# Performance work log

Measured on AMD Instinct MI355X. Metric: run time of the kernel, lower is better.

Reference implementation:

```python
import jax, jax.numpy as jnp
import numpy as np

EMB = 1024
HEADS = 16
HEAD_DIM = EMB // HEADS
EPS = 1e-5


def layer_norm(x, scale, shift):
    mean = jnp.mean(x, axis=-1, keepdims=True)
    var = jnp.mean(jnp.square(x - mean), axis=-1, keepdims=True)  # unbiased=False
    return scale * ((x - mean) / jnp.sqrt(var + EPS)) + shift


def gelu_tanh(x):
    c = jnp.sqrt(jnp.asarray(2.0 / jnp.pi, x.dtype))
    return 0.5 * x * (1.0 + jnp.tanh(c * (x + 0.044715 * x * x * x)))


def setup_inputs() -> dict:
    key = jax.random.key(0)
    ks = jax.random.split(key, 12)
    s = 0.02
    B, S, D = 2, 2048, EMB
    return {
        "x": jax.random.normal(ks[0], (B, S, D), jnp.float32),
        "wq": jax.random.normal(ks[1], (D, D), jnp.float32) * s,
        "wk": jax.random.normal(ks[2], (D, D), jnp.float32) * s,
        "wv": jax.random.normal(ks[3], (D, D), jnp.float32) * s,
        "wo": jax.random.normal(ks[4], (D, D), jnp.float32) * s,
        "bo": jnp.zeros((D,), jnp.float32),
        "w1": jax.random.normal(ks[5], (D, 4 * D), jnp.float32) * s,
        "b1": jnp.zeros((4 * D,), jnp.float32),
        "w2": jax.random.normal(ks[6], (4 * D, D), jnp.float32) * s,
        "b2": jnp.zeros((D,), jnp.float32),
        "g1": jnp.ones((D,), jnp.float32),
        "s1": jnp.zeros((D,), jnp.float32),
        "g2": jnp.ones((D,), jnp.float32),
        "s2": jnp.zeros((D,), jnp.float32),
    }


def reference(x, wq, wk, wv, wo, bo, w1, b1, w2, b2, g1, s1, g2, s2):
    B, S, D = x.shape
    # --- attention sub-block ---
    h = layer_norm(x, g1, s1)
    q = (h @ wq).reshape(B, S, HEADS, HEAD_DIM).transpose(0, 2, 1, 3)  # [B,H,S,d]
    k = (h @ wk).reshape(B, S, HEADS, HEAD_DIM).transpose(0, 2, 1, 3)
    v = (h @ wv).reshape(B, S, HEADS, HEAD_DIM).transpose(0, 2, 1, 3)
    scores = jnp.einsum("bhqd,bhkd->bhqk", q, k)
    causal = jnp.tril(jnp.ones((S, S), bool))  # True = keep
    scores = jnp.where(causal, scores, -jnp.inf)
    attn = jax.nn.softmax(scores / jnp.sqrt(jnp.asarray(HEAD_DIM, x.dtype)), axis=-1)
    ctx = jnp.einsum("bhqk,bhkd->bhqd", attn, v).transpose(0, 2, 1, 3).reshape(B, S, D)
    x = x + (ctx @ wo + bo)
    # --- FFN sub-block ---
    h = layer_norm(x, g2, s2)
    h = gelu_tanh(h @ w1 + b1) @ w2 + b2
    return x + h
```

## Files before the change

kernel.cpp:

```cpp
#include <hip/hip_runtime.h>


typedef __attribute__((ext_vector_type(8))) short s16x8;
typedef __attribute__((ext_vector_type(4))) float f32x4;
typedef __attribute__((ext_vector_type(16))) float f32x16;
typedef unsigned short u16;
typedef unsigned int u32;

#define DEV static __device__ __forceinline__
#define MFMA16 __builtin_amdgcn_mfma_f32_16x16x32_bf16
#define MFMA32 __builtin_amdgcn_mfma_f32_32x32x16_bf16
#define GLOAD_LDS16(gp, lp)                                         \
  __builtin_amdgcn_global_load_lds(                                 \
      (const __attribute__((address_space(1))) void*)(gp),          \
      (__attribute__((address_space(3))) void*)(lp), 16, 0, 0)

DEV u16 f2bf(float f) {
  union { float f; unsigned u; } c; c.f = f;
  unsigned u = c.u;
  u += 0x7fff + ((u >> 16) & 1);
  return (u16)(u >> 16);
}

DEV u32 cvtpk(float lo, float hi) {
  u32 r;
  asm("v_cvt_pk_bf16_f32 %0, %1, %2" : "=v"(r) : "v"(lo), "v"(hi));
  return r;
}

DEV float gelu_tanh(float v) {
  const float c0 = 0.7978845608028654f;
  float u = c0 * (v + 0.044715f * v * v * v);
  return 0.5f * v * (1.0f + tanhf(u));
}

DEV s16x8 ld8(const u16* p) { return *(const s16x8*)p; }

__global__ __launch_bounds__(256) void tconv_kernel(
    const float* __restrict__ W, u16* __restrict__ Wt, int K, int N) {
  __shared__ u16 T[64][80];
  const int t = threadIdx.x;
  const int n0 = blockIdx.x * 64, k0 = blockIdx.y * 64;
  const int kr = t >> 4, nc = (t & 15) * 4;
#pragma unroll
  for (int p = 0; p < 4; ++p) {
    const int k = p * 16 + kr;
    float4 v = *(const float4*)(W + (size_t)(k0 + k) * N + n0 + nc);
    T[nc + 0][k] = f2bf(v.x);
    T[nc + 1][k] = f2bf(v.y);
    T[nc + 2][k] = f2bf(v.z);
    T[nc + 3][k] = f2bf(v.w);
  }
  __syncthreads();
  const int nr = t >> 2, kc = (t & 3) * 16;
  *(s16x8*)(Wt + (size_t)(n0 + nr) * K + k0 + kc) = *(const s16x8*)&T[nr][kc];
  *(s16x8*)(Wt + (size_t)(n0 + nr) * K + k0 + kc + 8) =
      *(const s16x8*)&T[nr][kc + 8];
}

__global__ __launch_bounds__(256) void ln_kernel(
    const float* __restrict__ x, const float* __restrict__ g,
    const float* __restrict__ b, u16* __restrict__ out) {
  const int row = blockIdx.x;
  const int t = threadIdx.x;
  const float* xr = x + (size_t)row * 1024;
  float4 v = *(const float4*)(xr + t * 4);
  float s = v.x + v.y + v.z + v.w;
  float ss = v.x * v.x + v.y * v.y + v.z * v.z + v.w * v.w;
#pragma unroll
  for (int off = 1; off < 64; off <<= 1) {
    s += __shfl_xor(s, off);
    ss += __shfl_xor(ss, off);
  }
  __shared__ float sb[4], ssb[4];
  const int w = t >> 6;
  if ((t & 63) == 0) { sb[w] = s; ssb[w] = ss; }
  __syncthreads();
  s = sb[0] + sb[1] + sb[2] + sb[3];
  ss = ssb[0] + ssb[1] + ssb[2] + ssb[3];
  const float mean = s * (1.0f / 1024.0f);
  const float var = ss * (1.0f / 1024.0f) - mean * mean;
  const float rstd = rsqrtf(var + 1e-5f);
  const int c = t * 4;
  ushort4 o;
  o.x = f2bf(g[c + 0] * ((v.x - mean) * rstd) + b[c + 0]);
  o.y = f2bf(g[c + 1] * ((v.y - mean) * rstd) + b[c + 1]);
  o.z = f2bf(g[c + 2] * ((v.z - mean) * rstd) + b[c + 2]);
  o.w = f2bf(g[c + 3] * ((v.w - mean) * rstd) + b[c + 3]);
  *(ushort4*)(out + (size_t)row * 1024 + c) = o;
}

DEV void gemm_stage(const u16* __restrict__ A, const u16* __restrict__ Bt,
                    int bm, int bn, int K, int kof, u16 (*Al)[32],
                    u16 (*Bl)[32], int w, int lane) {
  const int srow = lane >> 2;
  const int scol = ((lane & 3) ^ ((lane >> 3) & 3)) * 8;
#pragma unroll
  for (int p = 0; p < 2; ++p) {
    const int r0 = (w * 2 + p) * 16;
    GLOAD_LDS16(A + (size_t)(bm + r0 + srow) * K + kof + scol, &Al[r0][0]);
    GLOAD_LDS16(Bt + (size_t)(bn + r0 + srow) * K + kof + scol, &Bl[r0][0]);
  }
}

DEV void gemm_step(const u16 (*Al)[32], const u16 (*Bl)[32],
                   f32x4 (&acc)[4][4], int wm, int wn, int lr, int lg) {
  const int cs = (lg ^ ((lr >> 1) & 3)) * 8;
  s16x8 af[4], bf[4];
#pragma unroll
  for (int i = 0; i < 4; ++i) {
    af[i] = *(const s16x8*)&Al[wm + i * 16 + lr][cs];
    bf[i] = *(const s16x8*)&Bl[wn + i * 16 + lr][cs];
  }
#pragma unroll
  for (int i = 0; i < 4; ++i)
#pragma unroll
    for (int j = 0; j < 4; ++j)
      acc[i][j] = MFMA16(af[i], bf[j], acc[i][j], 0, 0, 0);
}

template <int EPI>
__global__ __launch_bounds__(256) void gemm_kernel(
    const u16* __restrict__ A, const u16* __restrict__ Bt,
    const float* __restrict__ bias, const float* __restrict__ res,
    void* __restrict__ Cv, int M, int N, int K) {
  __shared__ __align__(16) u16 Al[2][128][32];
  __shared__ __align__(16) u16 Bl[2][128][32];
  const int t = threadIdx.x;
  const int lane = t & 63, w = t >> 6;
  const int wm = (w >> 1) * 64, wn = (w & 1) * 64;
  int bid = blockIdx.y * gridDim.x + blockIdx.x;
  const int q8 = (gridDim.x * gridDim.y) >> 3;
  bid = (bid & 7) * q8 + (bid >> 3);
  const int bm = (bid / gridDim.x) * 128, bn = (bid % gridDim.x) * 128;
  const int lr = lane & 15, lg = lane >> 4;
  f32x4 acc[4][4] = {};
  const int nkt = K >> 5;

  gemm_stage(A, Bt, bm, bn, K, 0, Al[0], Bl[0], w, lane);
  __syncthreads();
  for (int kt = 0; kt < nkt - 1; ++kt) {
    const int cur = kt & 1;
    gemm_stage(A, Bt, bm, bn, K, (kt + 1) << 5, Al[cur ^ 1], Bl[cur ^ 1], w,
               lane);
    gemm_step(Al[cur], Bl[cur], acc, wm, wn, lr, lg);
    __syncthreads();
  }
  gemm_step(Al[(nkt - 1) & 1], Bl[(nkt - 1) & 1], acc, wm, wn, lr, lg);

#pragma unroll
  for (int i = 0; i < 4; ++i) {
    const int row = bm + wm + i * 16 + lg * 4;
#pragma unroll
    for (int j = 0; j < 4; ++j) {
      const int col = bn + wn + j * 16 + lr;
      if (EPI == 0) {
        const int bb = row >> 11, sloc = row & 2047;
        const int which = col >> 10, n = col & 1023;
        const int hh = n >> 6, dd = n & 63;
        u16* qbuf = (u16*)Cv;
        if (which == 2) {
          ushort4 o;
          o.x = f2bf(acc[i][j][0]); o.y = f2bf(acc[i][j][1]);
          o.z = f2bf(acc[i][j][2]); o.w = f2bf(acc[i][j][3]);
          *(ushort4*)(qbuf + 8388608 +
                      (size_t)((bb * 16 + hh) * 64 + dd) * 2048 + sloc) = o;
        } else {
          const float sc = (which == 0) ? 0.18033688011112042f : 1.0f;
          u16* dst = qbuf + (size_t)which * 4194304 +
                     ((size_t)(bb * 16 + hh) * 2048 + sloc) * 64 + dd;
#pragma unroll
          for (int e = 0; e < 4; ++e) dst[(size_t)e * 64] = f2bf(acc[i][j][e] * sc);
        }
      } else if (EPI == 1) {
        float* C = (float*)Cv;
        const float bs = bias[col];
#pragma unroll
        for (int e = 0; e < 4; ++e)
          C[(size_t)(row + e) * N + col] =
              acc[i][j][e] + bs + res[(size_t)(row + e) * N + col];
      } else {
        u16* C = (u16*)Cv;
        const float bs = bias[col];
#pragma unroll
        for (int e = 0; e < 4; ++e)
          C[(size_t)(row + e) * N + col] = f2bf(gelu_tanh(acc[i][j][e] + bs));
      }
    }
  }
}

DEV void g64_stage(const u16* __restrict__ A, const u16* __restrict__ Bt,
                   int bm, int bn, int K, int kof, u16 (*Al)[32],
                   u16 (*Bl)[32], int w, int lane) {
  const int srow = lane >> 2;
  const int scol = ((lane & 3) ^ ((lane >> 3) & 3)) * 8;
  const int r0 = w << 4;
  GLOAD_LDS16(A + (size_t)(bm + r0 + srow) * K + kof + scol, &Al[r0][0]);
  GLOAD_LDS16(Bt + (size_t)(bn + r0 + srow) * K + kof + scol, &Bl[r0][0]);
}

DEV void g64_step(const u16 (*Al)[32], const u16 (*Bl)[32],
                  f32x4 (&acc)[2][2], int wm, int wn, int lr, int lg) {
  const int cs = (lg ^ ((lr >> 1) & 3)) * 8;
  s16x8 af[2], bf[2];
#pragma unroll
  for (int i = 0; i < 2; ++i) {
    af[i] = *(const s16x8*)&Al[wm + i * 16 + lr][cs];
    bf[i] = *(const s16x8*)&Bl[wn + i * 16 + lr][cs];
  }
#pragma unroll
  for (int i = 0; i < 2; ++i)
#pragma unroll
    for (int j = 0; j < 2; ++j)
      acc[i][j] = MFMA16(af[i], bf[j], acc[i][j], 0, 0, 0);
}

template <int EPI>
__global__ __launch_bounds__(256) void gemm64_kernel(
    const u16* __restrict__ A, const u16* __restrict__ Bt,
    const float* __restrict__ bias, const float* __restrict__ res,
    void* __restrict__ Cv, int M, int N, int K) {
  __shared__ __align__(16) u16 Al[2][64][32];
  __shared__ __align__(16) u16 Bl[2][64][32];
  const int t = threadIdx.x;
  const int lane = t & 63, w = t >> 6;
  const int wm = (w >> 1) * 32, wn = (w & 1) * 32;
  int bid = blockIdx.y * gridDim.x + blockIdx.x;
  const int q8 = (gridDim.x * gridDim.y) >> 3;
  bid = (bid & 7) * q8 + (bid >> 3);
  const int bm = (bid / gridDim.x) * 64, bn = (bid % gridDim.x) * 64;
  const int lr = lane & 15, lg = lane >> 4;
  f32x4 acc[2][2] = {};
  const int nkt = K >> 5;

  g64_stage(A, Bt, bm, bn, K, 0, Al[0], Bl[0], w, lane);
  __syncthreads();
  for (int kt = 0; kt < nkt - 1; ++kt) {
    const int cur = kt & 1;
    g64_stage(A, Bt, bm, bn, K, (kt + 1) << 5, Al[cur ^ 1], Bl[cur ^ 1], w,
              lane);
    g64_step(Al[cur], Bl[cur], acc, wm, wn, lr, lg);
    __syncthreads();
  }
  g64_step(Al[(nkt - 1) & 1], Bl[(nkt - 1) & 1], acc, wm, wn, lr, lg);

#pragma unroll
  for (int i = 0; i < 2; ++i) {
    const int row = bm + wm + i * 16 + lg * 4;
#pragma unroll
    for (int j = 0; j < 2; ++j) {
      const int col = bn + wn + j * 16 + lr;
      if (EPI == 1) {
        float* C = (float*)Cv;
        const float bs = bias[col];
#pragma unroll
        for (int e = 0; e < 4; ++e)
          C[(size_t)(row + e) * N + col] =
              acc[i][j][e] + bs + res[(size_t)(row + e) * N + col];
      } else {
        u16* C = (u16*)Cv;
        const float bs = bias[col];
#pragma unroll
        for (int e = 0; e < 4; ++e)
          C[(size_t)(row + e) * N + col] = f2bf(gelu_tanh(acc[i][j][e] + bs));
      }
    }
  }
}

DEV void g256_stage(const u16* __restrict__ A, const u16* __restrict__ Bt,
                    int bm, int bn, int K, int kof, u16 (*Al)[32],
                    u16 (*Bl)[32], int w, int lane) {
  const int srow = lane >> 2;
  const int scol = ((lane & 3) ^ ((lane >> 3) & 3)) * 8;
#pragma unroll
  for (int c = 0; c < 2; ++c) {
    const int r0 = (w << 5) + (c << 4);
    GLOAD_LDS16(A + (size_t)(bm + r0 + srow) * K + kof + scol, &Al[r0][0]);
    GLOAD_LDS16(Bt + (size_t)(bn + r0 + srow) * K + kof + scol, &Bl[r0][0]);
  }
}

DEV void g256_step(const u16 (*Al)[32], const u16 (*Bl)[32],
                   f32x4 (&acc)[8][4], int wm, int wn, int lr, int lg) {
  const int cs = (lg ^ ((lr >> 1) & 3)) * 8;
  s16x8 af[8], bf[4];
#pragma unroll
  for (int i = 0; i < 8; ++i)
    af[i] = *(const s16x8*)&Al[wm + i * 16 + lr][cs];
#pragma unroll
  for (int j = 0; j < 4; ++j)
    bf[j] = *(const s16x8*)&Bl[wn + j * 16 + lr][cs];
#pragma unroll
  for (int i = 0; i < 8; ++i)
#pragma unroll
    for (int j = 0; j < 4; ++j)
      acc[i][j] = MFMA16(af[i], bf[j], acc[i][j], 0, 0, 0);
}

template <int EPI>
__global__ __launch_bounds__(512, 2) void gemm256_kernel(
    const u16* __restrict__ A, const u16* __restrict__ Bt,
    const float* __restrict__ bias, const float* __restrict__ res,
    void* __restrict__ Cv, int M, int N, int K) {
  __shared__ __align__(16) u16 Al[2][256][32];
  __shared__ __align__(16) u16 Bl[2][256][32];
  const int t = threadIdx.x;
  const int lane = t & 63, w = t >> 6;
  const int wm = (w >> 2) << 7;
  const int wn = (w & 3) << 6;
  int bid = blockIdx.y * gridDim.x + blockIdx.x;
  const int q8 = (gridDim.x * gridDim.y) >> 3;
  bid = (bid & 7) * q8 + (bid >> 3);
  const int bm = (bid / gridDim.x) << 8, bn = (bid % gridDim.x) << 8;
  const int lr = lane & 15, lg = lane >> 4;
  f32x4 acc[8][4] = {};
  const int nkt = K >> 5;

  g256_stage(A, Bt, bm, bn, K, 0, Al[0], Bl[0], w, lane);
  __syncthreads();
  for (int kt = 0; kt < nkt - 1; ++kt) {
    const int cur = kt & 1;
    g256_stage(A, Bt, bm, bn, K, (kt + 1) << 5, Al[cur ^ 1], Bl[cur ^ 1], w,
               lane);
    g256_step(Al[cur], Bl[cur], acc, wm, wn, lr, lg);
    __syncthreads();
  }
  g256_step(Al[(nkt - 1) & 1], Bl[(nkt - 1) & 1], acc, wm, wn, lr, lg);

#pragma unroll
  for (int i = 0; i < 8; ++i) {
    const int row = bm + wm + i * 16 + lg * 4;
#pragma unroll
    for (int j = 0; j < 4; ++j) {
      const int col = bn + wn + j * 16 + lr;
      if (EPI == 1) {
        float* C = (float*)Cv;
        const float bs = bias[col];
#pragma unroll
        for (int e = 0; e < 4; ++e)
          C[(size_t)(row + e) * N + col] =
              acc[i][j][e] + bs + res[(size_t)(row + e) * N + col];
      } else {
        u16* C = (u16*)Cv;
        const float bs = bias[col];
#pragma unroll
        for (int e = 0; e < 4; ++e)
          C[(size_t)(row + e) * N + col] = f2bf(gelu_tanh(acc[i][j][e] + bs));
      }
    }
  }
}

DEV float vmax16(const f32x16& v) {
  float a = fmaxf(v[0], v[1]), b = fmaxf(v[2], v[3]);
  float c = fmaxf(v[4], v[5]), d = fmaxf(v[6], v[7]);
  float e = fmaxf(v[8], v[9]), f = fmaxf(v[10], v[11]);
  float g = fmaxf(v[12], v[13]), h = fmaxf(v[14], v[15]);
  a = fmaxf(a, b); c = fmaxf(c, d); e = fmaxf(e, f); g = fmaxf(g, h);
  return fmaxf(fmaxf(a, c), fmaxf(e, g));
}
DEV float vsum16(const f32x16& v) {
  float a = v[0] + v[1], b = v[2] + v[3];
  float c = v[4] + v[5], d = v[6] + v[7];
  float e = v[8] + v[9], f = v[10] + v[11];
  float g = v[12] + v[13], h = v[14] + v[15];
  a += b; c += d; e += f; g += h;
  return (a + c) + (e + g);
}

struct A32 {
  s16x8 q[4];
  f32x16 o0, o1;
  float m, l;
};

template <int MODE>
DEV void body32(A32& st, int k0, const u16* Kb, const u16* Vb, int la,
                int hi) {
  s16x8 ka0[4], ka1[4];
#pragma unroll
  for (int c = 0; c < 4; ++c)
    ka0[c] = ld8(Kb + (size_t)(k0 + la) * 64 + c * 16 + hi * 8);
  if (MODE != 2)
#pragma unroll
    for (int c = 0; c < 4; ++c)
      ka1[c] = ld8(Kb + (size_t)(k0 + 32 + la) * 64 + c * 16 + hi * 8);
  f32x16 s0, s1;
#pragma unroll
  for (int r = 0; r < 16; ++r) { s0[r] = 0.f; s1[r] = 0.f; }
#pragma unroll
  for (int c = 0; c < 4; ++c) s0 = MFMA32(ka0[c], st.q[c], s0, 0, 0, 0);
  if (MODE != 2)
#pragma unroll
    for (int c = 0; c < 4; ++c) s1 = MFMA32(ka1[c], st.q[c], s1, 0, 0, 0);
  const int nkc = (MODE == 2) ? 2 : 4;
  s16x8 va0[4], va1[4];
#pragma unroll
  for (int kc = 0; kc < 4; ++kc)
    if (kc < nkc) {
      va0[kc] = ld8(Vb + (size_t)la * 2048 + k0 + kc * 16 + hi * 8);
      va1[kc] = ld8(Vb + (size_t)(32 + la) * 2048 + k0 + kc * 16 + hi * 8);
    }
  if (MODE == 1) {
#pragma unroll
    for (int r = 0; r < 16; ++r) {
      const int kl = (r & 3) + 8 * (r >> 2) + 4 * hi;
      if (kl > la) s1[r] = -INFINITY;
    }
  }
  if (MODE == 2) {
#pragma unroll
    for (int r = 0; r < 16; ++r) {
      const int kl = (r & 3) + 8 * (r >> 2) + 4 * hi;
      if (kl > la) s0[r] = -INFINITY;
    }
  }
  float mt = vmax16(s0);
  if (MODE != 2) mt = fmaxf(mt, vmax16(s1));
  mt = fmaxf(mt, __shfl_xor(mt, 32));
  const float mn = fmaxf(st.m, mt);
  const float sf = exp2f(st.m - mn);
#pragma unroll
  for (int r = 0; r < 16; ++r) s0[r] = exp2f(s0[r] - mn);
  if (MODE != 2)
#pragma unroll
    for (int r = 0; r < 16; ++r) s1[r] = exp2f(s1[r] - mn);
  float rs = vsum16(s0);
  if (MODE != 2) rs += vsum16(s1);
  rs += __shfl_xor(rs, 32);
  st.l = st.l * sf + rs;
  st.m = mn;
#pragma unroll
  for (int r = 0; r < 16; ++r) { st.o0[r] *= sf; st.o1[r] *= sf; }
  const int nh = (MODE == 2) ? 1 : 2;
#pragma unroll
  for (int half = 0; half < nh; ++half) {
    u32 w[8];
#pragma unroll
    for (int i = 0; i < 8; ++i)
      w[i] = half ? cvtpk(s1[2 * i], s1[2 * i + 1])
                  : cvtpk(s0[2 * i], s0[2 * i + 1]);
#pragma unroll
    for (int kp = 0; kp < 2; ++kp) {
      const u32 w0 = w[4 * kp + 0], w1 = w[4 * kp + 1];
      const u32 w2 = w[4 * kp + 2], w3 = w[4 * kp + 3];
      const u32 t0 = hi ? w0 : w2, t1 = hi ? w1 : w3;
      const u32 x0 = (u32)__shfl_xor((int)t0, 32);
      const u32 x1 = (u32)__shfl_xor((int)t1, 32);
      union { u32 u[4]; s16x8 v; } bb;
      bb.u[0] = hi ? x0 : w0;
      bb.u[1] = hi ? x1 : w1;
      bb.u[2] = hi ? w2 : x0;
      bb.u[3] = hi ? w3 : x1;
      const int kc = half * 2 + kp;
      st.o0 = MFMA32(va0[kc], bb.v, st.o0, 0, 0, 0);
      st.o1 = MFMA32(va1[kc], bb.v, st.o1, 0, 0, 0);
    }
  }
}

DEV void a32_init(A32& st, const u16* Qbase, int qs, int la, int hi) {
#pragma unroll
  for (int c = 0; c < 4; ++c)
    st.q[c] = ld8(Qbase + (size_t)(qs + la) * 64 + c * 16 + hi * 8);
#pragma unroll
  for (int r = 0; r < 16; ++r) { st.o0[r] = 0.f; st.o1[r] = 0.f; }
  st.m = -INFINITY;
  st.l = 0.f;
}

DEV void a32_fin(const A32& st, u16* __restrict__ ctx, int bh, int qs, int la,
                 int hi) {
  const int bb = bh >> 4, hh = bh & 15;
  const float inv = 1.0f / st.l;
  u16* crow = ctx + (size_t)(bb * 2048 + qs + la) * 1024 + hh * 64;
#pragma unroll
  for (int r = 0; r < 16; r += 2) {
    const int d = (r & 3) + 8 * (r >> 2) + 4 * hi;
    *(u32*)(crow + d) = cvtpk(st.o0[r] * inv, st.o0[r + 1] * inv);
    *(u32*)(crow + 32 + d) = cvtpk(st.o1[r] * inv, st.o1[r + 1] * inv);
  }
}

template <bool ODD>
DEV void chain_tail(A32& st, int nfull, int qs, const u16* Kb, const u16* Vb,
                    int la, int hi) {
  if (ODD) body32<1>(st, nfull * 64, Kb, Vb, la, hi);
  else     body32<2>(st, qs, Kb, Vb, la, hi);
}

__global__ __launch_bounds__(64) void attn_kernel(
    const u16* __restrict__ Qg, const u16* __restrict__ Kg,
    const u16* __restrict__ Vt, u16* __restrict__ ctx) {
  const int lane = threadIdx.x & 63;
  const int la = lane & 31, hi = lane >> 5;
  const int tA = blockIdx.x;
  const int bh = blockIdx.y;
  const int tB = 63 - tA;
  const int qsA = tA * 32, qsB = tB * 32;
  const int nfA = tA >> 1, nfB = tB >> 1;
  const size_t baseK = (size_t)bh * 2048 * 64;
  const size_t baseV = (size_t)bh * 64 * 2048;
  const u16* Kb = Kg + baseK;
  const u16* Vb = Vt + baseV;

  A32 A, B;
  a32_init(A, Qg + baseK, qsA, la, hi);
  a32_init(B, Qg + baseK, qsB, la, hi);

  for (int kt = 0; kt < nfA; ++kt) {
    body32<0>(B, kt * 64, Kb, Vb, la, hi);
    body32<0>(A, kt * 64, Kb, Vb, la, hi);
  }
  body32<0>(B, nfA * 64, Kb, Vb, la, hi);
  if (tA & 1) chain_tail<true>(A, nfA, qsA, Kb, Vb, la, hi);
  else        chain_tail<false>(A, nfA, qsA, Kb, Vb, la, hi);
  a32_fin(A, ctx, bh, qsA, la, hi);

  for (int kt = nfA + 1; kt < nfB; ++kt)
    body32<0>(B, kt * 64, Kb, Vb, la, hi);
  if (tB & 1) chain_tail<true>(B, nfB, qsB, Kb, Vb, la, hi);
  else        chain_tail<false>(B, nfB, qsB, Kb, Vb, la, hi);
  a32_fin(B, ctx, bh, qsB, la, hi);
}

extern "C" void kernel_launch(void* const* d_in, const int* in_sizes, int n_in,
                              void* d_out, int out_size, void* d_ws,
                              size_t ws_size, hipStream_t stream) {
  const float* x  = (const float*)d_in[0];
  const float* wq = (const float*)d_in[1];
  const float* wk = (const float*)d_in[2];
  const float* wv = (const float*)d_in[3];
  const float* wo = (const float*)d_in[4];
  const float* bo = (const float*)d_in[5];
  const float* w1 = (const float*)d_in[6];
  const float* b1 = (const float*)d_in[7];
  const float* w2 = (const float*)d_in[8];
  const float* b2 = (const float*)d_in[9];
  const float* g1 = (const float*)d_in[10];
  const float* s1 = (const float*)d_in[11];
  const float* g2 = (const float*)d_in[12];
  const float* s2 = (const float*)d_in[13];
  float* out = (float*)d_out;

  const size_t MB = (size_t)1 << 20;
  char* p = (char*)d_ws;
  u16* hb    = (u16*)(p + 0 * MB);
  u16* qbuf  = (u16*)(p + 8 * MB);
  u16* ctxb  = (u16*)(p + 32 * MB);
  float* x2  = (float*)(p + 40 * MB);
  u16* h2b   = (u16*)(p + 56 * MB);
  u16* qkvw  = (u16*)(p + 64 * MB);
  u16* wot   = (u16*)(p + 70 * MB);
  u16* w1t   = (u16*)(p + 72 * MB);
  u16* w2t   = (u16*)(p + 80 * MB);
  u16* gb    = (u16*)(p + 0 * MB);

  const dim3 blk(256);
  tconv_kernel<<<dim3(16, 16), blk, 0, stream>>>(wq, qkvw, 1024, 1024);
  tconv_kernel<<<dim3(16, 16), blk, 0, stream>>>(wk, qkvw + 1048576, 1024, 1024);
  tconv_kernel<<<dim3(16, 16), blk, 0, stream>>>(wv, qkvw + 2097152, 1024, 1024);
  tconv_kernel<<<dim3(16, 16), blk, 0, stream>>>(wo, wot, 1024, 1024);
  tconv_kernel<<<dim3(64, 16), blk, 0, stream>>>(w1, w1t, 1024, 4096);
  tconv_kernel<<<dim3(16, 64), blk, 0, stream>>>(w2, w2t, 4096, 1024);

  ln_kernel<<<4096, blk, 0, stream>>>(x, g1, s1, hb);
  gemm_kernel<0><<<dim3(24, 32), blk, 0, stream>>>(hb, qkvw, nullptr, nullptr,
                                                   qbuf, 4096, 3072, 1024);
  attn_kernel<<<dim3(32, 32), dim3(64), 0, stream>>>(
      qbuf, qbuf + 4194304, qbuf + 8388608, ctxb);
  gemm64_kernel<1><<<dim3(16, 64), blk, 0, stream>>>(ctxb, wot, bo, x, x2,
                                                     4096, 1024, 1024);
  ln_kernel<<<4096, blk, 0, stream>>>(x2, g2, s2, h2b);
  gemm256_kernel<2><<<dim3(16, 16), dim3(512), 0, stream>>>(
      h2b, w1t, b1, nullptr, gb, 4096, 4096, 1024);
  gemm64_kernel<1><<<dim3(16, 64), blk, 0, stream>>>(gb, w2t, b2, x2, out,
                                                     4096, 1024, 4096);
}
```

Baseline: 302.5 us.

## Triple-buffer GEMM pipelines, merge weight conversions, lazy softmax rescale

```diff
diff --git a/kernel.cpp b/kernel.cpp
--- a/kernel.cpp
+++ b/kernel.cpp
@@ -14,6 +14,7 @@
   __builtin_amdgcn_global_load_lds(                                 \
       (const __attribute__((address_space(1))) void*)(gp),          \
       (__attribute__((address_space(3))) void*)(lp), 16, 0, 0)
+#define WAIT_VM(N) asm volatile("s_waitcnt vmcnt(" #N ")" ::: "memory")
 
 DEV u16 f2bf(float f) {
   union { float f; unsigned u; } c; c.f = f;
@@ -36,11 +37,10 @@
 
 DEV s16x8 ld8(const u16* p) { return *(const s16x8*)p; }
 
-__global__ __launch_bounds__(256) void tconv_kernel(
-    const float* __restrict__ W, u16* __restrict__ Wt, int K, int N) {
+DEV void tconv_tile(const float* __restrict__ W, u16* __restrict__ Wt, int K,
+                    int N, int bx, int by, int t) {
   __shared__ u16 T[64][80];
-  const int t = threadIdx.x;
-  const int n0 = blockIdx.x * 64, k0 = blockIdx.y * 64;
+  const int n0 = bx * 64, k0 = by * 64;
   const int kr = t >> 4, nc = (t & 15) * 4;
 #pragma unroll
   for (int p = 0; p < 4; ++p) {
@@ -56,6 +56,29 @@
   *(s16x8*)(Wt + (size_t)(n0 + nr) * K + k0 + kc) = *(const s16x8*)&T[nr][kc];
   *(s16x8*)(Wt + (size_t)(n0 + nr) * K + k0 + kc + 8) =
       *(const s16x8*)&T[nr][kc + 8];
+}
+
+__global__ __launch_bounds__(256) void tconv_all(
+    const float* __restrict__ wq, const float* __restrict__ wk,
+    const float* __restrict__ wv, const float* __restrict__ wo,
+    const float* __restrict__ w1, const float* __restrict__ w2,
+    u16* __restrict__ qkvw, u16* __restrict__ wot, u16* __restrict__ w1t,
+    u16* __restrict__ w2t) {
+  const int idx = blockIdx.x, t = threadIdx.x;
+  if (idx < 768) {
+    const int which = idx >> 8, r = idx & 255;
+    const float* W = which == 0 ? wq : (which == 1 ? wk : wv);
+    tconv_tile(W, qkvw + which * 1048576, 1024, 1024, r & 15, r >> 4, t);
+  } else if (idx < 1024) {
+    const int r = idx - 768;
+    tconv_tile(wo, wot, 1024, 1024, r & 15, r >> 4, t);
+  } else if (idx < 2048) {
+    const int r = idx - 1024;
+    tconv_tile(w1, w1t, 1024, 4096, r & 63, r >> 6, t);
+  } else {
+    const int r = idx - 2048;
+    tconv_tile(w2, w2t, 4096, 1024, r & 15, r >> 4, t);
+  }
 }
 
 __global__ __launch_bounds__(256) void ln_kernel(
@@ -90,9 +113,9 @@
   *(ushort4*)(out + (size_t)row * 1024 + c) = o;
 }
 
-DEV void gemm_stage(const u16* __restrict__ A, const u16* __restrict__ Bt,
-                    int bm, int bn, int K, int kof, u16 (*Al)[32],
-                    u16 (*Bl)[32], int w, int lane) {
+DEV void stage128(const u16* __restrict__ A, const u16* __restrict__ Bt,
+                  int bm, int bn, int K, int kof, u16 (*Al)[32],
+                  u16 (*Bl)[32], int w, int lane) {
   const int srow = lane >> 2;
   const int scol = ((lane & 3) ^ ((lane >> 3) & 3)) * 8;
 #pragma unroll
@@ -103,8 +126,8 @@
   }
 }
 
-DEV void gemm_step(const u16 (*Al)[32], const u16 (*Bl)[32],
-                   f32x4 (&acc)[4][4], int wm, int wn, int lr, int lg) {
+DEV void step128(const u16 (*Al)[32], const u16 (*Bl)[32],
+                 f32x4 (&acc)[4][4], int wm, int wn, int lr, int lg) {
   const int cs = (lg ^ ((lr >> 1) & 3)) * 8;
   s16x8 af[4], bf[4];
 #pragma unroll
@@ -120,12 +143,12 @@
 }
 
 template <int EPI>
-__global__ __launch_bounds__(256) void gemm_kernel(
+__global__ __launch_bounds__(256) void pipe128_kernel(
     const u16* __restrict__ A, const u16* __restrict__ Bt,
     const float* __restrict__ bias, const float* __restrict__ res,
     void* __restrict__ Cv, int M, int N, int K) {
-  __shared__ __align__(16) u16 Al[2][128][32];
-  __shared__ __align__(16) u16 Bl[2][128][32];
+  __shared__ __align__(16) u16 Al[3][128][32];
+  __shared__ __align__(16) u16 Bl[3][128][32];
   const int t = threadIdx.x;
   const int lane = t & 63, w = t >> 6;
   const int wm = (w >> 1) * 64, wn = (w & 1) * 64;
@@ -137,16 +160,18 @@
   f32x4 acc[4][4] = {};
   const int nkt = K >> 5;
 
-  gemm_stage(A, Bt, bm, bn, K, 0, Al[0], Bl[0], w, lane);
-  __syncthreads();
-  for (int kt = 0; kt < nkt - 1; ++kt) {
-    const int cur = kt & 1;
-    gemm_stage(A, Bt, bm, bn, K, (kt + 1) << 5, Al[cur ^ 1], Bl[cur ^ 1], w,
-               lane);
-    gemm_step(Al[cur], Bl[cur], acc, wm, wn, lr, lg);
-    __syncthreads();
-  }
-  gemm_step(Al[(nkt - 1) & 1], Bl[(nkt - 1) & 1], acc, wm, wn, lr, lg);
+  stage128(A, Bt, bm, bn, K, 0, Al[0], Bl[0], w, lane);
+  stage128(A, Bt, bm, bn, K, 32, Al[1], Bl[1], w, lane);
+  for (int kt = 0; kt < nkt; ++kt) {
+    if (kt == nkt - 1) WAIT_VM(0);
+    else               WAIT_VM(4);
+    __builtin_amdgcn_s_barrier();
+    if (kt + 2 < nkt) {
+      const int nb = (kt + 2) % 3;
+      stage128(A, Bt, bm, bn, K, (kt + 2) << 5, Al[nb], Bl[nb], w, lane);
+    }
+    step128(Al[kt % 3], Bl[kt % 3], acc, wm, wn, lr, lg);
+  }
 
 #pragma unroll
   for (int i = 0; i < 4; ++i) {
@@ -172,13 +197,6 @@
 #pragma unroll
           for (int e = 0; e < 4; ++e) dst[(size_t)e * 64] = f2bf(acc[i][j][e] * sc);
         }
-      } else if (EPI == 1) {
-        float* C = (float*)Cv;
-        const float bs = bias[col];
-#pragma unroll
-        for (int e = 0; e < 4; ++e)
-          C[(size_t)(row + e) * N + col] =
-              acc[i][j][e] + bs + res[(size_t)(row + e) * N + col];
       } else {
         u16* C = (u16*)Cv;
         const float bs = bias[col];
@@ -190,9 +208,9 @@
   }
 }
 
-DEV void g64_stage(const u16* __restrict__ A, const u16* __restrict__ Bt,
-                   int bm, int bn, int K, int kof, u16 (*Al)[32],
-                   u16 (*Bl)[32], int w, int lane) {
+DEV void stage64(const u16* __restrict__ A, const u16* __restrict__ Bt,
+                 int bm, int bn, int K, int kof, u16 (*Al)[32],
+                 u16 (*Bl)[32], int w, int lane) {
   const int srow = lane >> 2;
   const int scol = ((lane & 3) ^ ((lane >> 3) & 3)) * 8;
   const int r0 = w << 4;
@@ -200,8 +218,8 @@
   GLOAD_LDS16(Bt + (size_t)(bn + r0 + srow) * K + kof + scol, &Bl[r0][0]);
 }
 
-DEV void g64_step(const u16 (*Al)[32], const u16 (*Bl)[32],
-                  f32x4 (&acc)[2][2], int wm, int wn, int lr, int lg) {
+DEV void step64(const u16 (*Al)[32], const u16 (*Bl)[32],
+                f32x4 (&acc)[2][2], int wm, int wn, int lr, int lg) {
   const int cs = (lg ^ ((lr >> 1) & 3)) * 8;
   s16x8 af[2], bf[2];
 #pragma unroll
@@ -216,13 +234,12 @@
       acc[i][j] = MFMA16(af[i], bf[j], acc[i][j], 0, 0, 0);
 }
 
-template <int EPI>
-__global__ __launch_bounds__(256) void gemm64_kernel(
+__global__ __launch_bounds__(256) void pipe64_kernel(
     const u16* __restrict__ A, const u16* __restrict__ Bt,
     const float* __restrict__ bias, const float* __restrict__ res,
-    void* __restrict__ Cv, int M, int N, int K) {
-  __shared__ __align__(16) u16 Al[2][64][32];
-  __shared__ __align__(16) u16 Bl[2][64][32];
+    float* __restrict__ C, int M, int N, int K) {
+  __shared__ __align__(16) u16 Al[3][64][32];
+  __shared__ __align__(16) u16 Bl[3][64][32];
   const int t = threadIdx.x;
   const int lane = t & 63, w = t >> 6;
   const int wm = (w >> 1) * 32, wn = (w & 1) * 32;
@@ -234,16 +251,18 @@
   f32x4 acc[2][2] = {};
   const int nkt = K >> 5;
 
-  g64_stage(A, Bt, bm, bn, K, 0, Al[0], Bl[0], w, lane);
-  __syncthreads();
-  for (int kt = 0; kt < nkt - 1; ++kt) {
-    const int cur = kt & 1;
-    g64_stage(A, Bt, bm, bn, K, (kt + 1) << 5, Al[cur ^ 1], Bl[cur ^ 1], w,
-              lane);
-    g64_step(Al[cur], Bl[cur], acc, wm, wn, lr, lg);
-    __syncthreads();
-  }
-  g64_step(Al[(nkt - 1) & 1], Bl[(nkt - 1) & 1], acc, wm, wn, lr, lg);
+  stage64(A, Bt, bm, bn, K, 0, Al[0], Bl[0], w, lane);
+  stage64(A, Bt, bm, bn, K, 32, Al[1], Bl[1], w, lane);
+  for (int kt = 0; kt < nkt; ++kt) {
+    if (kt == nkt - 1) WAIT_VM(0);
+    else               WAIT_VM(2);
+    __builtin_amdgcn_s_barrier();
+    if (kt + 2 < nkt) {
+      const int nb = (kt + 2) % 3;
+      stage64(A, Bt, bm, bn, K, (kt + 2) << 5, Al[nb], Bl[nb], w, lane);
+    }
+    step64(Al[kt % 3], Bl[kt % 3], acc, wm, wn, lr, lg);
+  }
 
 #pragma unroll
   for (int i = 0; i < 2; ++i) {
@@ -251,104 +270,11 @@
 #pragma unroll
     for (int j = 0; j < 2; ++j) {
       const int col = bn + wn + j * 16 + lr;
-      if (EPI == 1) {
-        float* C = (float*)Cv;
-        const float bs = bias[col];
-#pragma unroll
-        for (int e = 0; e < 4; ++e)
-          C[(size_t)(row + e) * N + col] =
-              acc[i][j][e] + bs + res[(size_t)(row + e) * N + col];
-      } else {
-        u16* C = (u16*)Cv;
-        const float bs = bias[col];
-#pragma unroll
-        for (int e = 0; e < 4; ++e)
-          C[(size_t)(row + e) * N + col] = f2bf(gelu_tanh(acc[i][j][e] + bs));
-      }
-    }
-  }
-}
-
-DEV void g256_stage(const u16* __restrict__ A, const u16* __restrict__ Bt,
-                    int bm, int bn, int K, int kof, u16 (*Al)[32],
-                    u16 (*Bl)[32], int w, int lane) {
-  const int srow = lane >> 2;
-  const int scol = ((lane & 3) ^ ((lane >> 3) & 3)) * 8;
-#pragma unroll
-  for (int c = 0; c < 2; ++c) {
-    const int r0 = (w << 5) + (c << 4);
-    GLOAD_LDS16(A + (size_t)(bm + r0 + srow) * K + kof + scol, &Al[r0][0]);
-    GLOAD_LDS16(Bt + (size_t)(bn + r0 + srow) * K + kof + scol, &Bl[r0][0]);
-  }
-}
-
-DEV void g256_step(const u16 (*Al)[32], const u16 (*Bl)[32],
-                   f32x4 (&acc)[8][4], int wm, int wn, int lr, int lg) {
-  const int cs = (lg ^ ((lr >> 1) & 3)) * 8;
-  s16x8 af[8], bf[4];
-#pragma unroll
-  for (int i = 0; i < 8; ++i)
-    af[i] = *(const s16x8*)&Al[wm + i * 16 + lr][cs];
-#pragma unroll
-  for (int j = 0; j < 4; ++j)
-    bf[j] = *(const s16x8*)&Bl[wn + j * 16 + lr][cs];
-#pragma unroll
-  for (int i = 0; i < 8; ++i)
-#pragma unroll
-    for (int j = 0; j < 4; ++j)
-      acc[i][j] = MFMA16(af[i], bf[j], acc[i][j], 0, 0, 0);
-}
-
-template <int EPI>
-__global__ __launch_bounds__(512, 2) void gemm256_kernel(
-    const u16* __restrict__ A, const u16* __restrict__ Bt,
-    const float* __restrict__ bias, const float* __restrict__ res,
-    void* __restrict__ Cv, int M, int N, int K) {
-  __shared__ __align__(16) u16 Al[2][256][32];
-  __shared__ __align__(16) u16 Bl[2][256][32];
-  const int t = threadIdx.x;
-  const int lane = t & 63, w = t >> 6;
-  const int wm = (w >> 2) << 7;
-  const int wn = (w & 3) << 6;
-  int bid = blockIdx.y * gridDim.x + blockIdx.x;
-  const int q8 = (gridDim.x * gridDim.y) >> 3;
-  bid = (bid & 7) * q8 + (bid >> 3);
-  const int bm = (bid / gridDim.x) << 8, bn = (bid % gridDim.x) << 8;
-  const int lr = lane & 15, lg = lane >> 4;
-  f32x4 acc[8][4] = {};
-  const int nkt = K >> 5;
-
-  g256_stage(A, Bt, bm, bn, K, 0, Al[0], Bl[0], w, lane);
-  __syncthreads();
-  for (int kt = 0; kt < nkt - 1; ++kt) {
-    const int cur = kt & 1;
-    g256_stage(A, Bt, bm, bn, K, (kt + 1) << 5, Al[cur ^ 1], Bl[cur ^ 1], w,
-               lane);
-    g256_step(Al[cur], Bl[cur], acc, wm, wn, lr, lg);
-    __syncthreads();
-  }
-  g256_step(Al[(nkt - 1) & 1], Bl[(nkt - 1) & 1], acc, wm, wn, lr, lg);
-
-#pragma unroll
-  for (int i = 0; i < 8; ++i) {
-    const int row = bm + wm + i * 16 + lg * 4;
-#pragma unroll
-    for (int j = 0; j < 4; ++j) {
-      const int col = bn + wn + j * 16 + lr;
-      if (EPI == 1) {
-        float* C = (float*)Cv;
-        const float bs = bias[col];
-#pragma unroll
-        for (int e = 0; e < 4; ++e)
-          C[(size_t)(row + e) * N + col] =
-              acc[i][j][e] + bs + res[(size_t)(row + e) * N + col];
-      } else {
-        u16* C = (u16*)Cv;
-        const float bs = bias[col];
-#pragma unroll
-        for (int e = 0; e < 4; ++e)
-          C[(size_t)(row + e) * N + col] = f2bf(gelu_tanh(acc[i][j][e] + bs));
-      }
+      const float bs = bias[col];
+#pragma unroll
+      for (int e = 0; e < 4; ++e)
+        C[(size_t)(row + e) * N + col] =
+            acc[i][j][e] + bs + res[(size_t)(row + e) * N + col];
     }
   }
 }
@@ -420,8 +346,9 @@
   float mt = vmax16(s0);
   if (MODE != 2) mt = fmaxf(mt, vmax16(s1));
   mt = fmaxf(mt, __shfl_xor(mt, 32));
-  const float mn = fmaxf(st.m, mt);
-  const float sf = exp2f(st.m - mn);
+  const bool skip = __all(mt <= st.m + 8.0f) != 0;
+  const float mn = skip ? st.m : fmaxf(st.m, mt);
+  const float sf = skip ? 1.0f : exp2f(st.m - mn);
 #pragma unroll
   for (int r = 0; r < 16; ++r) s0[r] = exp2f(s0[r] - mn);
   if (MODE != 2)
@@ -430,10 +357,12 @@
   float rs = vsum16(s0);
   if (MODE != 2) rs += vsum16(s1);
   rs += __shfl_xor(rs, 32);
-  st.l = st.l * sf + rs;
+  st.l = skip ? (st.l + rs) : (st.l * sf + rs);
   st.m = mn;
-#pragma unroll
-  for (int r = 0; r < 16; ++r) { st.o0[r] *= sf; st.o1[r] *= sf; }
+  if (!skip) {
+#pragma unroll
+    for (int r = 0; r < 16; ++r) { st.o0[r] *= sf; st.o1[r] *= sf; }
+  }
   const int nh = (MODE == 2) ? 1 : 2;
 #pragma unroll
   for (int half = 0; half < nh; ++half) {
@@ -559,23 +488,18 @@
   u16* gb    = (u16*)(p + 0 * MB);
 
   const dim3 blk(256);
-  tconv_kernel<<<dim3(16, 16), blk, 0, stream>>>(wq, qkvw, 1024, 1024);
-  tconv_kernel<<<dim3(16, 16), blk, 0, stream>>>(wk, qkvw + 1048576, 1024, 1024);
-  tconv_kernel<<<dim3(16, 16), blk, 0, stream>>>(wv, qkvw + 2097152, 1024, 1024);
-  tconv_kernel<<<dim3(16, 16), blk, 0, stream>>>(wo, wot, 1024, 1024);
-  tconv_kernel<<<dim3(64, 16), blk, 0, stream>>>(w1, w1t, 1024, 4096);
-  tconv_kernel<<<dim3(16, 64), blk, 0, stream>>>(w2, w2t, 4096, 1024);
-
+  tconv_all<<<dim3(3072), blk, 0, stream>>>(wq, wk, wv, wo, w1, w2, qkvw, wot,
+                                            w1t, w2t);
   ln_kernel<<<4096, blk, 0, stream>>>(x, g1, s1, hb);
-  gemm_kernel<0><<<dim3(24, 32), blk, 0, stream>>>(hb, qkvw, nullptr, nullptr,
-                                                   qbuf, 4096, 3072, 1024);
+  pipe128_kernel<0><<<dim3(24, 32), blk, 0, stream>>>(
+      hb, qkvw, nullptr, nullptr, qbuf, 4096, 3072, 1024);
   attn_kernel<<<dim3(32, 32), dim3(64), 0, stream>>>(
       qbuf, qbuf + 4194304, qbuf + 8388608, ctxb);
-  gemm64_kernel<1><<<dim3(16, 64), blk, 0, stream>>>(ctxb, wot, bo, x, x2,
-                                                     4096, 1024, 1024);
+  pipe64_kernel<<<dim3(16, 64), blk, 0, stream>>>(ctxb, wot, bo, x, x2, 4096,
+                                                  1024, 1024);
   ln_kernel<<<4096, blk, 0, stream>>>(x2, g2, s2, h2b);
-  gemm256_kernel<2><<<dim3(16, 16), dim3(512), 0, stream>>>(
+  pipe128_kernel<2><<<dim3(32, 32), blk, 0, stream>>>(
       h2b, w1t, b1, nullptr, gb, 4096, 4096, 1024);
-  gemm64_kernel<1><<<dim3(16, 64), blk, 0, stream>>>(gb, w2t, b2, x2, out,
-                                                     4096, 1024, 4096);
-}
+  pipe64_kernel<<<dim3(16, 64), blk, 0, stream>>>(gb, w2t, b2, x2, out, 4096,
+                                                  1024, 4096);
+}
```

Result: no change. 302.8 us (+0.1%).
